# Performance work log

Hardware: AMD Instinct MI355X
Metric: run time of the kernel (lower is better)

## Reference

```python
import jax, jax.numpy as jnp
import numpy as np

B, C, H, W = 8, 512, 64, 128
K = 19          # num_classes
BH, BW = 2, 4   # bin_size
N = BH * BW     # bin_num
CI = C // 2     # feat_inner


def setup_inputs() -> dict:
    ks = jax.random.split(jax.random.key(0), 10)
    def nrm(k, shape, s=0.02):
        return jax.random.normal(k, shape, jnp.float32) * s
    return {
        "x": jax.random.normal(ks[0], (B, C, H, W), jnp.float32),
        "conv_cam_w": nrm(ks[1], (K, C)),
        "conv_cam_b": jnp.zeros((K,), jnp.float32),
        "gcn_w1": nrm(ks[2], (N, N), 0.1),
        "gcn_a": jnp.full((N,), 0.25, jnp.float32),
        "gcn_w2": nrm(ks[3], (C, C)),
        "fuse_w": nrm(ks[4], (1, N), 0.1),
        "fuse_b": jnp.zeros((1,), jnp.float32),
        "relu_a": jnp.full((1,), 0.25, jnp.float32),
        "q_w": nrm(ks[5], (CI, C)),
        "q_b": jnp.zeros((CI,), jnp.float32),
        "k_w": nrm(ks[6], (CI, C)),
        "k_b": jnp.zeros((CI,), jnp.float32),
        "v_w": nrm(ks[7], (CI, C)),
        "v_b": jnp.zeros((CI,), jnp.float32),
        "out_w": nrm(ks[8], (C, CI)),
        "bn_gamma": jnp.ones((C,), jnp.float32),
        "bn_beta": jnp.zeros((C,), jnp.float32),
        "out_a": jnp.full((C,), 0.25, jnp.float32),
    }


def _prelu(x, a):
    return jnp.maximum(x, 0) + a * jnp.minimum(x, 0)


def _split(t):
    # [b, cc, H, W] -> [b, N, rh*rw, cc]  (patch_split)
    b, cc = t.shape[0], t.shape[1]
    rh, rw = H // BH, W // BW
    t = t.reshape(b, cc, BH, rh, BW, rw).transpose(0, 2, 4, 3, 5, 1)
    return t.reshape(b, N, rh * rw, cc)


def _caam(x, conv_cam_w, conv_cam_b, gcn_w1, gcn_a, gcn_w2, fuse_w, fuse_b,
          relu_a, q_w, q_b, k_w, k_b, v_w, v_b, out_w, bn_gamma, bn_beta, out_a):
    b = x.shape[0]
    rh, rw = H // BH, W // BW
    # CAM (1x1 conv) + adaptive avg pool to bins + sigmoid
    cam = jnp.einsum('bchw,kc->bkhw', x, conv_cam_w) + conv_cam_b[None, :, None, None]
    cls_score = jax.nn.sigmoid(cam.reshape(b, K, BH, rh, BW, rw).mean((3, 5)))  # [b,K,BH,BW]
    cam_p = _split(cam)   # [b,N,P,K]
    x_p = _split(x)       # [b,N,P,C]
    bin_conf = cls_score.reshape(b, K, N).transpose(0, 2, 1)[..., None]  # [b,N,K,1]
    pix_conf = jax.nn.softmax(cam_p, axis=2)
    local = jnp.einsum('bnpk,bnpc->bnkc', pix_conf, x_p) * bin_conf  # [b,N,K,C]
    # GCN: conv1 over bin dim, PReLU(residual), Linear over channels
    t = jnp.einsum('nm,bmkc->bnkc', gcn_w1, local)
    t = _prelu(t + local, gcn_a[None, :, None, None])
    local = jnp.einsum('bnkc,dc->bnkd', t, gcn_w2)
    # fuse bins -> single global descriptor, PReLU(1)
    glob = jnp.einsum('on,bnkc->bokc', fuse_w, local) + fuse_b[None, :, None, None]  # [b,1,K,C]
    glob = _prelu(glob[:, 0], relu_a[0])  # [b,K,C]
    # QKV attention over bins (key/value over K class slots)
    q = jnp.einsum('bnpc,ic->bnpi', x_p, q_w) + q_b       # [b,N,P,CI]
    key = jnp.einsum('bnkc,ic->bnki', local, k_w) + k_b   # [b,N,K,CI]
    val = jnp.einsum('bkc,ic->bki', glob, v_w) + v_b      # [b,K,CI] (shared across bins)
    aff = jax.nn.softmax(jnp.einsum('bnpi,bnki->bnpk', q, key), axis=-1)
    out = jnp.einsum('bnpk,bki->bnpi', aff, val)          # [b,N,P,CI]
    # patch_recover -> [b,CI,H,W]
    out = out.reshape(b, BH, BW, rh, rw, CI).transpose(0, 5, 1, 3, 2, 4).reshape(b, CI, H, W)
    # conv_out: 1x1 conv (no bias) + BatchNorm2d (batch stats) + PReLU(C)
    y = jnp.einsum('bihw,ci->bchw', out, out_w)
    mu = y.mean((0, 2, 3), keepdims=True)
    var = y.var((0, 2, 3), keepdims=True)
    y = (y - mu) * jax.lax.rsqrt(var + 1e-5)
    y = y * bn_gamma[None, :, None, None] + bn_beta[None, :, None, None]
    y = _prelu(y, out_a[None, :, None, None])
    return x + y


def reference(x, conv_cam_w, conv_cam_b, gcn_w1, gcn_a, gcn_w2, fuse_w, fuse_b,
              relu_a, q_w, q_b, k_w, k_b, v_w, v_b, out_w, bn_gamma, bn_beta, out_a):
    return _caam(x, conv_cam_w, conv_cam_b, gcn_w1, gcn_a, gcn_w2, fuse_w, fuse_b,
                 relu_a, q_w, q_b, k_w, k_b, v_w, v_b, out_w, bn_gamma, bn_beta, out_a)
```

## Files before the change

### kernel.cpp

```cpp
#include <hip/hip_runtime.h>
#include <cstdint>
#include <cstddef>

#define B_ 8
#define C_ 512
#define H_ 64
#define W_ 128
#define HW_ 8192
#define K_ 19
#define N_ 8
#define P_ 1024
#define CI_ 256

typedef unsigned short u16;
typedef unsigned int u32;
typedef __attribute__((ext_vector_type(8))) short bf16x8;
typedef __attribute__((ext_vector_type(4))) float f32x4;

__device__ __forceinline__ u16 f2bf(float f) {
  u32 u = __float_as_uint(f);
  u32 r = (u + 0x7FFFu + ((u >> 16) & 1u)) >> 16;
  return (u16)r;
}
__device__ __forceinline__ float bf2f(u16 h) {
  return __uint_as_float(((u32)h) << 16);
}

__device__ __forceinline__ void gload16(const u16* g, u16* l) {
  __builtin_amdgcn_global_load_lds(
      (const __attribute__((address_space(1))) unsigned int*)g,
      (__attribute__((address_space(3))) unsigned int*)l, 16, 0, 0);
}

__device__ __forceinline__ void stage128(const u16* __restrict__ src, size_t ld, int k0,
                                         u16* lds, int wave, int lane) {
  int rsub = lane >> 3;
  int swz = ((lane & 7) ^ rsub) << 3;
#pragma unroll
  for (int i = 0; i < 4; i++) {
    int rowbase = wave * 8 + i * 32;
    gload16(src + (size_t)(rowbase + rsub) * ld + k0 + swz, lds + rowbase * 64);
  }
}
__device__ __forceinline__ void stage32(const u16* __restrict__ src, size_t ld, int k0,
                                        u16* lds, int wave, int lane) {
  int rsub = lane >> 3;
  int swz = ((lane & 7) ^ rsub) << 3;
  int rowbase = wave * 8;
  gload16(src + (size_t)(rowbase + rsub) * ld + k0 + swz, lds + rowbase * 64);
}
__device__ __forceinline__ bf16x8 frag(const u16* lds, int row, int qbyte) {
  return *(const bf16x8*)((const char*)lds + row * 128 + (qbyte ^ ((row & 7) << 4)));
}

__device__ __forceinline__ float blockSum256(float v, float* red4) {
#pragma unroll
  for (int o = 32; o > 0; o >>= 1) v += __shfl_down(v, o, 64);
  __syncthreads();
  if ((threadIdx.x & 63) == 0) red4[threadIdx.x >> 6] = v;
  __syncthreads();
  return red4[0] + red4[1] + red4[2] + red4[3];
}

__device__ __forceinline__ float blockMax256(float v, float* red4) {
#pragma unroll
  for (int o = 32; o > 0; o >>= 1) v = fmaxf(v, __shfl_down(v, o, 64));
  __syncthreads();
  if ((threadIdx.x & 63) == 0) red4[threadIdx.x >> 6] = v;
  __syncthreads();
  return fmaxf(fmaxf(red4[0], red4[1]), fmaxf(red4[2], red4[3]));
}

__device__ __forceinline__ void cvt4(const float* __restrict__ s, u16* __restrict__ d, int i) {
  float4 v = *(const float4*)&s[(size_t)i * 4];
  ushort4 o;
  o.x = f2bf(v.x); o.y = f2bf(v.y); o.z = f2bf(v.z); o.w = f2bf(v.w);
  *(ushort4*)&d[(size_t)i * 4] = o;
}

__global__ __launch_bounds__(256) void xpose_prep_kernel(const float* __restrict__ x,
                                                         u16* __restrict__ xt,
                                                         const float* __restrict__ qw,
                                                         const float* __restrict__ ow,
                                                         const float* __restrict__ kw,
                                                         const float* __restrict__ gw2,
                                                         const float* __restrict__ camw,
                                                         u16* __restrict__ qwbf,
                                                         u16* __restrict__ owbf,
                                                         u16* __restrict__ kwbf,
                                                         u16* __restrict__ gw2bf,
                                                         u16* __restrict__ camwbf,
                                                         float* __restrict__ sums,
                                                         float* __restrict__ tpad) {
  __shared__ float tile[64][65];
  int bid = blockIdx.x;
  int tid = threadIdx.x;
  if (bid >= 8192) {
    int pb = bid - 8192;
    if (pb < 128) {
      cvt4(qw, qwbf, pb * 256 + tid);
    } else if (pb < 256) {
      cvt4(ow, owbf, (pb - 128) * 256 + tid);
    } else if (pb < 384) {
      cvt4(kw, kwbf, (pb - 256) * 256 + tid);
    } else if (pb < 640) {
      cvt4(gw2, gw2bf, (pb - 384) * 256 + tid);
    } else if (pb < 656) {
      int i = (pb - 640) * 256 + tid;
      if (i * 4 < K_ * C_) {
        cvt4(camw, camwbf, i);
      } else {
        ushort4 z; z.x = 0; z.y = 0; z.z = 0; z.w = 0;
        *(ushort4*)&camwbf[(size_t)i * 4] = z;
      }
    } else if (pb == 656) {
      float4 z; z.x = 0.f; z.y = 0.f; z.z = 0.f; z.w = 0.f;
      *(float4*)&sums[tid * 4] = z;
    } else {
      int i = (pb - 657) * 256 + tid;
      float4 z; z.x = 0.f; z.y = 0.f; z.z = 0.f; z.w = 0.f;
      *(float4*)&tpad[(size_t)i * 4] = z;
    }
    return;
  }
  int hw0 = (bid & 127) << 6;
  int c0 = ((bid >> 7) & 7) << 6;
  int b = bid >> 10;
  int r = tid >> 4;
  int col4 = (tid & 15) << 2;
  const float* xb = x + ((size_t)b * C_ + c0) * HW_ + hw0;
#pragma unroll
  for (int it = 0; it < 4; it++) {
    int rr = r + it * 16;
    float4 v = *(const float4*)&xb[(size_t)rr * HW_ + col4];
    tile[rr][col4 + 0] = v.x;
    tile[rr][col4 + 1] = v.y;
    tile[rr][col4 + 2] = v.z;
    tile[rr][col4 + 3] = v.w;
  }
  __syncthreads();
  u16* xo = xt + ((size_t)b * HW_ + hw0) * C_ + c0;
#pragma unroll
  for (int it = 0; it < 4; it++) {
    int hwr = r + it * 16;
    ushort4 o;
    o.x = f2bf(tile[col4 + 0][hwr]);
    o.y = f2bf(tile[col4 + 1][hwr]);
    o.z = f2bf(tile[col4 + 2][hwr]);
    o.w = f2bf(tile[col4 + 3][hwr]);
    *(ushort4*)&xo[(size_t)hwr * C_ + col4] = o;
  }
}

__global__ __launch_bounds__(256) void gemm_cam_kernel(const u16* __restrict__ A,
                                                       const u16* __restrict__ Bw,
                                                       const float* __restrict__ bias,
                                                       float* __restrict__ cam) {
  __shared__ __align__(16) u16 As[128 * 64];
  __shared__ __align__(16) u16 Bs[32 * 64];
  int b = blockIdx.y;
  int m0 = blockIdx.x * 128;
  int tid = threadIdx.x;
  int wave = tid >> 6, lane = tid & 63;
  int wm = wave * 32;
  int quad = lane >> 4, l16 = lane & 15;
  const u16* Ab = A + (size_t)b * HW_ * C_ + (size_t)m0 * C_;
  f32x4 acc[2][2] = {};
  for (int k0 = 0; k0 < C_; k0 += 64) {
    __syncthreads();
    stage128(Ab, C_, k0, As, wave, lane);
    stage32(Bw, C_, k0, Bs, wave, lane);
    __syncthreads();
#pragma unroll
    for (int kk = 0; kk < 2; kk++) {
      int qb_ = kk * 64 + quad * 16;
      bf16x8 af[2], bfv[2];
#pragma unroll
      for (int t = 0; t < 2; t++) {
        af[t] = frag(As, wm + t * 16 + l16, qb_);
        bfv[t] = frag(Bs, t * 16 + l16, qb_);
      }
#pragma unroll
      for (int tm = 0; tm < 2; tm++)
#pragma unroll
        for (int tn = 0; tn < 2; tn++)
          acc[tm][tn] = __builtin_amdgcn_mfma_f32_16x16x32_bf16(af[tm], bfv[tn], acc[tm][tn], 0, 0, 0);
    }
  }
  float* C = cam + (size_t)b * K_ * HW_;
#pragma unroll
  for (int tm = 0; tm < 2; tm++) {
    int mm = m0 + wm + tm * 16 + quad * 4;
#pragma unroll
    for (int tn = 0; tn < 2; tn++) {
      int nn = tn * 16 + l16;
      if (nn < K_) {
        float bv = bias[nn];
        f32x4 v = acc[tm][tn];
        v[0] += bv; v[1] += bv; v[2] += bv; v[3] += bv;
        *(f32x4*)&C[(size_t)nn * HW_ + mm] = v;
      }
    }
  }
}

__global__ __launch_bounds__(256) void softcls_kernel(const float* __restrict__ cam,
                                                      float* __restrict__ bconf,
                                                      float* __restrict__ pconf) {
  __shared__ float red4[4];
  int bid = blockIdx.x;
  int k = bid % 19;
  int n = (bid / 19) & 7;
  int b = bid / 152;
  int bh = n >> 2, bw = n & 3;
  const float* base = cam + ((size_t)b * K_ + k) * HW_ + (bh * 32) * W_ + bw * 32;
  float v[4];
  float s = 0.f, mx = -1e30f;
#pragma unroll
  for (int j = 0; j < 4; j++) {
    int p = threadIdx.x + j * 256;
    v[j] = base[(p >> 5) * W_ + (p & 31)];
    s += v[j];
    mx = fmaxf(mx, v[j]);
  }
  float tot = blockSum256(s, red4);
  if (threadIdx.x == 0) {
    float m = tot * (1.f / 1024.f);
    bconf[bid] = 1.f / (1.f + __expf(-m));
  }
  mx = blockMax256(mx, red4);
  float e[4];
  float se = 0.f;
#pragma unroll
  for (int j = 0; j < 4; j++) { e[j] = __expf(v[j] - mx); se += e[j]; }
  se = blockSum256(se, red4);
  float inv = 1.f / se;
  float* outp = pconf + (size_t)bid * P_;
#pragma unroll
  for (int j = 0; j < 4; j++) outp[threadIdx.x + j * 256] = e[j] * inv;
}

__global__ __launch_bounds__(256) void local_part_kernel(const u16* __restrict__ xt,
                                                         const float* __restrict__ pconf,
                                                         float* __restrict__ part) {
  __shared__ __align__(16) float pcl[19 * 256];
  int bid = blockIdx.x;
  int pq = bid & 3;
  int half = (bid >> 2) & 1;
  int n = (bid >> 3) & 7;
  int b = bid >> 6;
  int tid = threadIdx.x;
  int c = half * 256 + tid;
  int bh = n >> 2, bw = n & 3;
  const float* pcb = pconf + (size_t)((b * N_ + n) * K_) * P_ + pq * 256;
  for (int e = tid; e < 19 * 64; e += 256) {
    int k = e >> 6, q4 = e & 63;
    *(float4*)&pcl[k * 256 + q4 * 4] = *(const float4*)&pcb[(size_t)k * P_ + q4 * 4];
  }
  __syncthreads();
  float acc[K_];
#pragma unroll
  for (int k = 0; k < K_; k++) acc[k] = 0.f;
  const u16* xb = xt + (size_t)b * HW_ * C_ + c;
  for (int pl0 = 0; pl0 < 256; pl0 += 8) {
    float xv[8];
#pragma unroll
    for (int g = 0; g < 2; g++) {
      int p = pq * 256 + pl0 + g * 4;
      int hw = (bh * 32 + (p >> 5)) * W_ + bw * 32 + (p & 31);
      const u16* xr = xb + (size_t)hw * C_;
#pragma unroll
      for (int j = 0; j < 4; j++) xv[g * 4 + j] = bf2f(xr[(size_t)j * C_]);
    }
#pragma unroll
    for (int k = 0; k < K_; k++) {
      float4 p0 = *(const float4*)&pcl[k * 256 + pl0];
      float4 p1 = *(const float4*)&pcl[k * 256 + pl0 + 4];
      acc[k] += p0.x * xv[0] + p0.y * xv[1] + p0.z * xv[2] + p0.w * xv[3]
              + p1.x * xv[4] + p1.y * xv[5] + p1.z * xv[6] + p1.w * xv[7];
    }
  }
  int row = (b * N_ + n) * K_;
  float* pp = part + ((size_t)pq * 1216 + row) * C_ + c;
#pragma unroll
  for (int k = 0; k < K_; k++) pp[(size_t)k * C_] = acc[k];
}

__global__ __launch_bounds__(256) void t_kernel(const float* __restrict__ part,
                                                const float* __restrict__ bconf,
                                                const float* __restrict__ gw1,
                                                const float* __restrict__ ga,
                                                u16* __restrict__ tbuf) {
  __shared__ float gw1l[64];
  __shared__ float gal[8];
  __shared__ float bcl[8];
  int tid = threadIdx.x;
  int bid = blockIdx.x;
  int half = bid & 1;
  int rem = bid >> 1;
  int k = rem % 19;
  int b = rem / 19;
  if (tid < 64) gw1l[tid] = gw1[tid];
  if (tid < 8) {
    gal[tid] = ga[tid];
    bcl[tid] = bconf[(size_t)(b * 8 + tid) * 19 + k];
  }
  __syncthreads();
  int c = half * 256 + tid;
  float lm[8];
#pragma unroll
  for (int m = 0; m < 8; m++) {
    size_t off = ((size_t)(b * N_ + m) * K_ + k) * C_ + c;
    lm[m] = (part[off] + part[off + (size_t)1216 * 512] +
             part[off + (size_t)2 * 1216 * 512] + part[off + (size_t)3 * 1216 * 512]) * bcl[m];
  }
#pragma unroll
  for (int n = 0; n < 8; n++) {
    float v = lm[n];
#pragma unroll
    for (int m = 0; m < 8; m++) v += gw1l[n * 8 + m] * lm[m];
    float t = fmaxf(v, 0.f) + gal[n] * fminf(v, 0.f);
    tbuf[((size_t)((b * N_ + n) * K_ + k)) * C_ + c] = f2bf(t);
  }
}

template <int KDIM, int NDIM, bool BIAS>
__device__ __forceinline__ void gemm_small_body(int bidx,
                                                const u16* __restrict__ A,
                                                const u16* __restrict__ Bw,
                                                const float* __restrict__ bias,
                                                float* __restrict__ f32out,
                                                u16* __restrict__ bf16out,
                                                u16* As, u16* Bs) {
  constexpr int NT = NDIM / 128;
  int m0 = (bidx / NT) * 128;
  int n0 = (bidx % NT) * 128;
  int tid = threadIdx.x;
  int wave = tid >> 6, lane = tid & 63;
  int wm = (wave >> 1) * 64, wn = (wave & 1) * 64;
  int quad = lane >> 4, l16 = lane & 15;
  const u16* Ab = A + (size_t)m0 * KDIM;
  const u16* Bb = Bw + (size_t)n0 * KDIM;
  f32x4 acc[4][4] = {};
  for (int k0 = 0; k0 < KDIM; k0 += 64) {
    __syncthreads();
    stage128(Ab, KDIM, k0, As, wave, lane);
    stage128(Bb, KDIM, k0, Bs, wave, lane);
    __syncthreads();
#pragma unroll
    for (int kk = 0; kk < 2; kk++) {
      int qb_ = kk * 64 + quad * 16;
      bf16x8 af[4], bfv[4];
#pragma unroll
      for (int t = 0; t < 4; t++) {
        af[t] = frag(As, wm + t * 16 + l16, qb_);
        bfv[t] = frag(Bs, wn + t * 16 + l16, qb_);
      }
#pragma unroll
      for (int tm = 0; tm < 4; tm++)
#pragma unroll
        for (int tn = 0; tn < 4; tn++)
          acc[tm][tn] = __builtin_amdgcn_mfma_f32_16x16x32_bf16(af[tm], bfv[tn], acc[tm][tn], 0, 0, 0);
    }
  }
  float bv[4];
#pragma unroll
  for (int tn = 0; tn < 4; tn++)
    bv[tn] = BIAS ? bias[n0 + wn + tn * 16 + l16] : 0.f;
#pragma unroll
  for (int tm = 0; tm < 4; tm++) {
    int mm = m0 + wm + tm * 16 + quad * 4;
#pragma unroll
    for (int tn = 0; tn < 4; tn++) {
      int nn = n0 + wn + tn * 16 + l16;
#pragma unroll
      for (int reg = 0; reg < 4; reg++) {
        float v = acc[tm][tn][reg] + bv[tn];
        if (f32out) f32out[(size_t)(mm + reg) * NDIM + nn] = v;
        if (bf16out) bf16out[(size_t)(mm + reg) * NDIM + nn] = f2bf(v);
      }
    }
  }
}

template <int KDIM, int NDIM, bool BIAS>
__global__ __launch_bounds__(256) void gemm_small_kernel(const u16* __restrict__ A,
                                                         const u16* __restrict__ Bw,
                                                         const float* __restrict__ bias,
                                                         float* __restrict__ f32out,
                                                         u16* __restrict__ bf16out) {
  __shared__ __align__(16) u16 As[128 * 64];
  __shared__ __align__(16) u16 Bs[128 * 64];
  gemm_small_body<KDIM, NDIM, BIAS>(blockIdx.x, A, Bw, bias, f32out, bf16out, As, Bs);
}

__device__ __forceinline__ void glob_val_body(int bid,
                                              const float* __restrict__ locl2,
                                              const float* __restrict__ fw,
                                              const float* __restrict__ fb,
                                              const float* __restrict__ ra,
                                              const float* __restrict__ vw,
                                              const float* __restrict__ vb,
                                              float* __restrict__ valo,
                                              float* gl) {
  int k = bid % 19;
  int b = bid / 19;
  int tid = threadIdx.x;
  float fwr[8];
#pragma unroll
  for (int m = 0; m < 8; m++) fwr[m] = fw[m];
  float fbv = fb[0], rav = ra[0];
  const float* lb = locl2 + ((size_t)(b * N_) * K_ + k) * C_;
  for (int c = tid; c < C_; c += 256) {
    float v = fbv;
#pragma unroll
    for (int m = 0; m < 8; m++) v += fwr[m] * lb[(size_t)m * K_ * C_ + c];
    gl[c] = fmaxf(v, 0.f) + rav * fminf(v, 0.f);
  }
  __syncthreads();
  int i = tid;
  const float* wr = vw + (size_t)i * C_;
  float s = vb[i];
  for (int c4 = 0; c4 < C_; c4 += 4) {
    float4 wv = *(const float4*)&wr[c4];
    float4 tv = *(const float4*)&gl[c4];
    s += wv.x * tv.x + wv.y * tv.y + wv.z * tv.z + wv.w * tv.w;
  }
  valo[(size_t)bid * CI_ + i] = s;
}

__global__ __launch_bounds__(256) void small2_globval_kernel(const u16* __restrict__ A,
                                                             const u16* __restrict__ Bw,
                                                             const float* __restrict__ bias,
                                                             float* __restrict__ keyo,
                                                             const float* __restrict__ locl2,
                                                             const float* __restrict__ fw,
                                                             const float* __restrict__ fb,
                                                             const float* __restrict__ ra,
                                                             const float* __restrict__ vw,
                                                             const float* __restrict__ vb,
                                                             float* __restrict__ valo) {
  __shared__ __align__(16) u16 As[128 * 64];
  __shared__ __align__(16) u16 Bs[128 * 64];
  if (blockIdx.x < 20) {
    gemm_small_body<512, 256, true>(blockIdx.x, A, Bw, bias, keyo, nullptr, As, Bs);
  } else {
    glob_val_body(blockIdx.x - 20, locl2, fw, fb, ra, vw, vb, valo, (float*)As);
  }
}

template <int KDIM, int NDIM, bool TRANS_OUT, bool BIAS, bool OUTBF16, bool BNSTAT>
__global__ __launch_bounds__(256) void gemm_big_kernel(const u16* __restrict__ A,
                                                       const u16* __restrict__ Bw,
                                                       const float* __restrict__ bias,
                                                       void* __restrict__ Cout,
                                                       float* __restrict__ sums,
                                                       float* __restrict__ sumsq) {
  __shared__ __align__(16) u16 As[128 * 64];
  __shared__ __align__(16) u16 Bs[128 * 64];
  constexpr int NT = NDIM / 128;
  int b = blockIdx.y;
  int d = blockIdx.x;
  int xcd = d & 7;
  int j = d >> 3;
  int m0 = (xcd + 8 * (j / NT)) * 128;
  int n0 = (j % NT) * 128;
  int tid = threadIdx.x;
  int wave = tid >> 6, lane = tid & 63;
  int wm = (wave >> 1) * 64, wn = (wave & 1) * 64;
  int quad = lane >> 4, l16 = lane & 15;
  const u16* Ab = A + (size_t)b * 8192 * KDIM + (size_t)m0 * KDIM;
  const u16* Bb = Bw + (size_t)n0 * KDIM;
  f32x4 acc[4][4] = {};
  for (int k0 = 0; k0 < KDIM; k0 += 64) {
    __syncthreads();
    stage128(Ab, KDIM, k0, As, wave, lane);
    stage128(Bb, KDIM, k0, Bs, wave, lane);
    __syncthreads();
#pragma unroll
    for (int kk = 0; kk < 2; kk++) {
      int qb_ = kk * 64 + quad * 16;
      bf16x8 af[4], bfv[4];
#pragma unroll
      for (int t = 0; t < 4; t++) {
        af[t] = frag(As, wm + t * 16 + l16, qb_);
        bfv[t] = frag(Bs, wn + t * 16 + l16, qb_);
      }
#pragma unroll
      for (int tm = 0; tm < 4; tm++)
#pragma unroll
        for (int tn = 0; tn < 4; tn++)
          acc[tm][tn] = __builtin_amdgcn_mfma_f32_16x16x32_bf16(af[tm], bfv[tn], acc[tm][tn], 0, 0, 0);
    }
  }
  if constexpr (!TRANS_OUT) {
    float bv[4];
#pragma unroll
    for (int tn = 0; tn < 4; tn++)
      bv[tn] = BIAS ? bias[n0 + wn + tn * 16 + l16] : 0.f;
#pragma unroll
    for (int tm = 0; tm < 4; tm++) {
      int mm = m0 + wm + tm * 16 + quad * 4;
#pragma unroll
      for (int tn = 0; tn < 4; tn++) {
        int nn = n0 + wn + tn * 16 + l16;
        if constexpr (OUTBF16) {
          u16* C = (u16*)Cout + (size_t)b * 8192 * NDIM;
#pragma unroll
          for (int reg = 0; reg < 4; reg++)
            C[(size_t)(mm + reg) * NDIM + nn] = f2bf(acc[tm][tn][reg] + bv[tn]);
        } else {
          float* C = (float*)Cout + (size_t)b * 8192 * NDIM;
#pragma unroll
          for (int reg = 0; reg < 4; reg++)
            C[(size_t)(mm + reg) * NDIM + nn] = acc[tm][tn][reg] + bv[tn];
        }
      }
    }
  } else {
    float* C = (float*)Cout + (size_t)b * NDIM * 8192;
#pragma unroll
    for (int tm = 0; tm < 4; tm++) {
      int mm = m0 + wm + tm * 16 + quad * 4;
#pragma unroll
      for (int tn = 0; tn < 4; tn++) {
        int nn = n0 + wn + tn * 16 + l16;
        *(f32x4*)&C[(size_t)nn * 8192 + mm] = acc[tm][tn];
      }
    }
    if constexpr (BNSTAT) {
#pragma unroll
      for (int tn = 0; tn < 4; tn++) {
        int nn = n0 + wn + tn * 16 + l16;
        float s = 0.f, q = 0.f;
#pragma unroll
        for (int tm = 0; tm < 4; tm++)
#pragma unroll
          for (int reg = 0; reg < 4; reg++) {
            float v = acc[tm][tn][reg];
            s += v;
            q += v * v;
          }
        s += __shfl_xor(s, 16, 64); q += __shfl_xor(q, 16, 64);
        s += __shfl_xor(s, 32, 64); q += __shfl_xor(q, 32, 64);
        if (quad == 0) {
          atomicAdd(&sums[nn], s);
          atomicAdd(&sumsq[nn], q);
        }
      }
    }
  }
}

__global__ __launch_bounds__(256) void attn2_kernel(const u16* __restrict__ q,
                                                    const float* __restrict__ keyo,
                                                    const float* __restrict__ valo,
                                                    u16* __restrict__ obuf) {
  __shared__ float keyl[19 * 256];
  __shared__ float vall[19 * 256];
  __shared__ float aff[128 * 20];
  int bid = blockIdx.x;
  int rg = bid & 7;
  int n = (bid >> 3) & 7;
  int b = bid >> 6;
  int bh = n >> 2, bw = n & 3;
  int tid = threadIdx.x;
  const float* ksrc = keyo + (size_t)((b * 8 + n) * 19) * 256;
  for (int e = tid; e < 19 * 256; e += 256) keyl[e] = ksrc[e];
  __syncthreads();
  if (tid < 128) {
    int r = rg * 4 + (tid >> 5);
    int wc = tid & 31;
    int hw = (bh * 32 + r) * W_ + bw * 32 + wc;
    const u16* qr = q + ((size_t)b * HW_ + hw) * 256;
    float acc[19];
#pragma unroll
    for (int k = 0; k < 19; k++) acc[k] = 0.f;
    for (int i0 = 0; i0 < 256; i0 += 8) {
      uint4 v = *(const uint4*)&qr[i0];
      float f0 = __uint_as_float((v.x & 0xFFFFu) << 16);
      float f1 = __uint_as_float(v.x & 0xFFFF0000u);
      float f2 = __uint_as_float((v.y & 0xFFFFu) << 16);
      float f3 = __uint_as_float(v.y & 0xFFFF0000u);
      float f4 = __uint_as_float((v.z & 0xFFFFu) << 16);
      float f5 = __uint_as_float(v.z & 0xFFFF0000u);
      float f6 = __uint_as_float((v.w & 0xFFFFu) << 16);
      float f7 = __uint_as_float(v.w & 0xFFFF0000u);
#pragma unroll
      for (int k = 0; k < 19; k++) {
        const float* kr = &keyl[k * 256 + i0];
        acc[k] += f0 * kr[0] + f1 * kr[1] + f2 * kr[2] + f3 * kr[3] +
                  f4 * kr[4] + f5 * kr[5] + f6 * kr[6] + f7 * kr[7];
      }
    }
    float mx = -1e30f;
#pragma unroll
    for (int k = 0; k < 19; k++) mx = fmaxf(mx, acc[k]);
    float se = 0.f;
#pragma unroll
    for (int k = 0; k < 19; k++) { acc[k] = __expf(acc[k] - mx); se += acc[k]; }
    float inv = 1.f / se;
#pragma unroll
    for (int k = 0; k < 19; k++) aff[tid * 20 + k] = acc[k] * inv;
  } else {
    const float* vsrc = valo + (size_t)b * 19 * 256;
    for (int e = tid - 128; e < 19 * 256; e += 128) vall[e] = vsrc[e];
  }
  __syncthreads();
  int px = tid & 127;
  int ih = (tid >> 7) * 128;
  int r3 = rg * 4 + (px >> 5);
  int wc3 = px & 31;
  int hw3 = (bh * 32 + r3) * W_ + bw * 32 + wc3;
  float av[19];
#pragma unroll
  for (int k = 0; k < 19; k++) av[k] = aff[px * 20 + k];
  u16* ob = obuf + ((size_t)b * HW_ + hw3) * 256 + ih;
  for (int i0 = 0; i0 < 128; i0 += 16) {
    float o16[16];
#pragma unroll
    for (int j = 0; j < 16; j++) o16[j] = 0.f;
#pragma unroll
    for (int k = 0; k < 19; k++) {
      float a = av[k];
      const float* vr = &vall[k * 256 + ih + i0];
#pragma unroll
      for (int j = 0; j < 16; j++) o16[j] += a * vr[j];
    }
    uint4 w0, w1;
    w0.x = (u32)f2bf(o16[0]) | ((u32)f2bf(o16[1]) << 16);
    w0.y = (u32)f2bf(o16[2]) | ((u32)f2bf(o16[3]) << 16);
    w0.z = (u32)f2bf(o16[4]) | ((u32)f2bf(o16[5]) << 16);
    w0.w = (u32)f2bf(o16[6]) | ((u32)f2bf(o16[7]) << 16);
    w1.x = (u32)f2bf(o16[8]) | ((u32)f2bf(o16[9]) << 16);
    w1.y = (u32)f2bf(o16[10]) | ((u32)f2bf(o16[11]) << 16);
    w1.z = (u32)f2bf(o16[12]) | ((u32)f2bf(o16[13]) << 16);
    w1.w = (u32)f2bf(o16[14]) | ((u32)f2bf(o16[15]) << 16);
    *(uint4*)&ob[i0] = w0;
    *(uint4*)&ob[i0 + 8] = w1;
  }
}

__global__ __launch_bounds__(256) void final_kernel(const float* __restrict__ x,
                                                    const float* __restrict__ sums,
                                                    const float* __restrict__ sumsq,
                                                    const float* __restrict__ gamma,
                                                    const float* __restrict__ beta,
                                                    const float* __restrict__ oa,
                                                    float* __restrict__ out) {
  size_t base = (size_t)blockIdx.x * 4096 + threadIdx.x * 4;
  int c = (int)((base >> 13) & 511);
  const float inv_cnt = 1.f / 65536.f;
  float mu = sums[c] * inv_cnt;
  float var = sumsq[c] * inv_cnt - mu * mu;
  float iv = rsqrtf(var + 1e-5f);
  float sc = gamma[c] * iv;
  float sh = beta[c] - mu * sc;
  float a = oa[c];
#pragma unroll
  for (int jj = 0; jj < 4; jj++) {
    size_t idx = base + (size_t)jj * 1024;
    float4 y = *(float4*)&out[idx];
    float4 xv = *(const float4*)&x[idx];
    float4 r;
    float t;
    t = y.x * sc + sh; r.x = xv.x + fmaxf(t, 0.f) + a * fminf(t, 0.f);
    t = y.y * sc + sh; r.y = xv.y + fmaxf(t, 0.f) + a * fminf(t, 0.f);
    t = y.z * sc + sh; r.z = xv.z + fmaxf(t, 0.f) + a * fminf(t, 0.f);
    t = y.w * sc + sh; r.w = xv.w + fmaxf(t, 0.f) + a * fminf(t, 0.f);
    *(float4*)&out[idx] = r;
  }
}

extern "C" void kernel_launch(void* const* d_in, const int* in_sizes, int n_in,
                              void* d_out, int out_size, void* d_ws, size_t ws_size,
                              hipStream_t stream) {
  const float* x     = (const float*)d_in[0];
  const float* camw  = (const float*)d_in[1];
  const float* camb  = (const float*)d_in[2];
  const float* gw1   = (const float*)d_in[3];
  const float* ga    = (const float*)d_in[4];
  const float* gw2   = (const float*)d_in[5];
  const float* fw    = (const float*)d_in[6];
  const float* fb    = (const float*)d_in[7];
  const float* ra    = (const float*)d_in[8];
  const float* qw    = (const float*)d_in[9];
  const float* qb    = (const float*)d_in[10];
  const float* kw    = (const float*)d_in[11];
  const float* kb    = (const float*)d_in[12];
  const float* vw    = (const float*)d_in[13];
  const float* vb    = (const float*)d_in[14];
  const float* ow    = (const float*)d_in[15];
  const float* gamma = (const float*)d_in[16];
  const float* beta  = (const float*)d_in[17];
  const float* oa    = (const float*)d_in[18];
  float* out = (float*)d_out;
  float* ws = (float*)d_ws;

  float* cam    = ws;
  float* bconf  = cam + 1245184;
  float* pconf  = bconf + 2048;
  float* locl   = pconf + 1245184;
  float* locl2f = locl + 622592;
  float* keyo   = locl2f + 655360;
  float* valo   = keyo + 327680;
  float* sums   = valo + 38912;
  float* sumsq  = sums + 512;
  float* scale  = sumsq + 512;
  float* shift  = scale + 512;
  u16* qwbf   = (u16*)(shift + 512);
  u16* owbf   = qwbf + 131072;
  u16* kwbf   = owbf + 131072;
  u16* gw2bf  = kwbf + 131072;
  u16* camwbf = gw2bf + 262144;
  u16* tbuf   = camwbf + 16384;
  u16* l2bf   = tbuf + 655360;
  u16* xt     = l2bf + 655360;
  u16* obuf   = xt;
  u16* qbuf   = xt + 33554432;
  float* part = (float*)qbuf;

  xpose_prep_kernel<<<8865, 256, 0, stream>>>(x, xt, qw, ow, kw, gw2, camw,
                                              qwbf, owbf, kwbf, gw2bf, camwbf,
                                              sums, (float*)(tbuf + 1216 * 512));
  gemm_cam_kernel<<<dim3(64, 8), 256, 0, stream>>>(xt, camwbf, camb, cam);
  softcls_kernel<<<1216, 256, 0, stream>>>(cam, bconf, pconf);
  local_part_kernel<<<512, 256, 0, stream>>>(xt, pconf, part);
  t_kernel<<<304, 256, 0, stream>>>(part, bconf, gw1, ga, tbuf);
  gemm_small_kernel<512, 512, false>
      <<<40, 256, 0, stream>>>(tbuf, gw2bf, nullptr, locl2f, l2bf);
  small2_globval_kernel<<<172, 256, 0, stream>>>(l2bf, kwbf, kb, keyo,
                                                 locl2f, fw, fb, ra, vw, vb, valo);
  gemm_big_kernel<512, 256, false, true, true, false>
      <<<dim3(128, 8), 256, 0, stream>>>(xt, qwbf, qb, qbuf, nullptr, nullptr);
  attn2_kernel<<<512, 256, 0, stream>>>(qbuf, keyo, valo, obuf);
  gemm_big_kernel<256, 512, true, false, false, true>
      <<<dim3(256, 8), 256, 0, stream>>>(obuf, owbf, nullptr, out, sums, sumsq);
  final_kernel<<<8192, 256, 0, stream>>>(x, sums, sumsq, gamma, beta, oa, out);
}
```

Baseline: 549.3 us.

## Split Q-projection GEMM across small kernels and store conv_out result as bf16

The standalone Q-projection GEMM is cut into four slices of two batches each. Each slice is appended as extra blocks to one of the small, under-occupied kernels in the middle of the pipeline (local_part, t, small gemm, key/globval), so its work overlaps with that serial chain. Separately, the conv_out GEMM now writes y as bf16 instead of fp32, halving that intermediate's write and read traffic for final_kernel. BN statistics are still taken from the fp32 accumulators, but y itself is rounded to bf16 before normalisation, and the workspace layout moves part further out to make room.

```diff
diff --git a/kernel.cpp b/kernel.cpp
--- a/kernel.cpp
+++ b/kernel.cpp
@@ -240,11 +240,135 @@
   for (int j = 0; j < 4; j++) outp[threadIdx.x + j * 256] = e[j] * inv;
 }
 
-__global__ __launch_bounds__(256) void local_part_kernel(const u16* __restrict__ xt,
-                                                         const float* __restrict__ pconf,
-                                                         float* __restrict__ part) {
-  __shared__ __align__(16) float pcl[19 * 256];
-  int bid = blockIdx.x;
+template <int KDIM, int NDIM, bool TRANS_OUT, bool BIAS, bool OUTBF16, bool BNSTAT>
+__device__ __forceinline__ void gemm_big_body(int bx, int b,
+                                              const u16* __restrict__ A,
+                                              const u16* __restrict__ Bw,
+                                              const float* __restrict__ bias,
+                                              void* __restrict__ Cout,
+                                              float* __restrict__ sums,
+                                              float* __restrict__ sumsq,
+                                              u16* As, u16* Bs) {
+  constexpr int NT = NDIM / 128;
+  int xcd = bx & 7;
+  int j = bx >> 3;
+  int m0 = (xcd + 8 * (j / NT)) * 128;
+  int n0 = (j % NT) * 128;
+  int tid = threadIdx.x;
+  int wave = tid >> 6, lane = tid & 63;
+  int wm = (wave >> 1) * 64, wn = (wave & 1) * 64;
+  int quad = lane >> 4, l16 = lane & 15;
+  const u16* Ab = A + (size_t)b * 8192 * KDIM + (size_t)m0 * KDIM;
+  const u16* Bb = Bw + (size_t)n0 * KDIM;
+  f32x4 acc[4][4] = {};
+  for (int k0 = 0; k0 < KDIM; k0 += 64) {
+    __syncthreads();
+    stage128(Ab, KDIM, k0, As, wave, lane);
+    stage128(Bb, KDIM, k0, Bs, wave, lane);
+    __syncthreads();
+#pragma unroll
+    for (int kk = 0; kk < 2; kk++) {
+      int qb_ = kk * 64 + quad * 16;
+      bf16x8 af[4], bfv[4];
+#pragma unroll
+      for (int t = 0; t < 4; t++) {
+        af[t] = frag(As, wm + t * 16 + l16, qb_);
+        bfv[t] = frag(Bs, wn + t * 16 + l16, qb_);
+      }
+#pragma unroll
+      for (int tm = 0; tm < 4; tm++)
+#pragma unroll
+        for (int tn = 0; tn < 4; tn++)
+          acc[tm][tn] = __builtin_amdgcn_mfma_f32_16x16x32_bf16(af[tm], bfv[tn], acc[tm][tn], 0, 0, 0);
+    }
+  }
+  if constexpr (!TRANS_OUT) {
+    float bv[4];
+#pragma unroll
+    for (int tn = 0; tn < 4; tn++)
+      bv[tn] = BIAS ? bias[n0 + wn + tn * 16 + l16] : 0.f;
+#pragma unroll
+    for (int tm = 0; tm < 4; tm++) {
+      int mm = m0 + wm + tm * 16 + quad * 4;
+#pragma unroll
+      for (int tn = 0; tn < 4; tn++) {
+        int nn = n0 + wn + tn * 16 + l16;
+        if constexpr (OUTBF16) {
+          u16* C = (u16*)Cout + (size_t)b * 8192 * NDIM;
+#pragma unroll
+          for (int reg = 0; reg < 4; reg++)
+            C[(size_t)(mm + reg) * NDIM + nn] = f2bf(acc[tm][tn][reg] + bv[tn]);
+        } else {
+          float* C = (float*)Cout + (size_t)b * 8192 * NDIM;
+#pragma unroll
+          for (int reg = 0; reg < 4; reg++)
+            C[(size_t)(mm + reg) * NDIM + nn] = acc[tm][tn][reg] + bv[tn];
+        }
+      }
+    }
+  } else {
+#pragma unroll
+    for (int tm = 0; tm < 4; tm++) {
+      int mm = m0 + wm + tm * 16 + quad * 4;
+#pragma unroll
+      for (int tn = 0; tn < 4; tn++) {
+        int nn = n0 + wn + tn * 16 + l16;
+        if constexpr (OUTBF16) {
+          u16* C = (u16*)Cout + (size_t)b * NDIM * 8192;
+          ushort4 o;
+          o.x = f2bf(acc[tm][tn][0]);
+          o.y = f2bf(acc[tm][tn][1]);
+          o.z = f2bf(acc[tm][tn][2]);
+          o.w = f2bf(acc[tm][tn][3]);
+          *(ushort4*)&C[(size_t)nn * 8192 + mm] = o;
+        } else {
+          float* C = (float*)Cout + (size_t)b * NDIM * 8192;
+          *(f32x4*)&C[(size_t)nn * 8192 + mm] = acc[tm][tn];
+        }
+      }
+    }
+    if constexpr (BNSTAT) {
+#pragma unroll
+      for (int tn = 0; tn < 4; tn++) {
+        int nn = n0 + wn + tn * 16 + l16;
+        float s = 0.f, q = 0.f;
+#pragma unroll
+        for (int tm = 0; tm < 4; tm++)
+#pragma unroll
+          for (int reg = 0; reg < 4; reg++) {
+            float v = acc[tm][tn][reg];
+            s += v;
+            q += v * v;
+          }
+        s += __shfl_xor(s, 16, 64); q += __shfl_xor(q, 16, 64);
+        s += __shfl_xor(s, 32, 64); q += __shfl_xor(q, 32, 64);
+        if (quad == 0) {
+          atomicAdd(&sums[nn], s);
+          atomicAdd(&sumsq[nn], q);
+        }
+      }
+    }
+  }
+}
+
+template <int KDIM, int NDIM, bool TRANS_OUT, bool BIAS, bool OUTBF16, bool BNSTAT>
+__global__ __launch_bounds__(256) void gemm_big_kernel(const u16* __restrict__ A,
+                                                       const u16* __restrict__ Bw,
+                                                       const float* __restrict__ bias,
+                                                       void* __restrict__ Cout,
+                                                       float* __restrict__ sums,
+                                                       float* __restrict__ sumsq) {
+  __shared__ __align__(16) u16 As[128 * 64];
+  __shared__ __align__(16) u16 Bs[128 * 64];
+  gemm_big_body<KDIM, NDIM, TRANS_OUT, BIAS, OUTBF16, BNSTAT>(
+      blockIdx.x, blockIdx.y, A, Bw, bias, Cout, sums, sumsq, As, Bs);
+}
+
+__device__ __forceinline__ void local_part_body(int bid,
+                                                const u16* __restrict__ xt,
+                                                const float* __restrict__ pconf,
+                                                float* __restrict__ part,
+                                                float* pcl) {
   int pq = bid & 3;
   int half = (bid >> 2) & 1;
   int n = (bid >> 3) & 7;
@@ -286,16 +410,46 @@
   for (int k = 0; k < K_; k++) pp[(size_t)k * C_] = acc[k];
 }
 
-__global__ __launch_bounds__(256) void t_kernel(const float* __restrict__ part,
-                                                const float* __restrict__ bconf,
-                                                const float* __restrict__ gw1,
-                                                const float* __restrict__ ga,
-                                                u16* __restrict__ tbuf) {
-  __shared__ float gw1l[64];
-  __shared__ float gal[8];
-  __shared__ float bcl[8];
+__global__ __launch_bounds__(256) void local_part_q_kernel(const u16* __restrict__ xt,
+                                                           const float* __restrict__ pconf,
+                                                           float* __restrict__ part,
+                                                           const u16* __restrict__ qwbf,
+                                                           const float* __restrict__ qb,
+                                                           u16* __restrict__ qbuf) {
+  __shared__ __align__(16) u16 smem[16384];
+  int bid = blockIdx.x;
+  if (bid < 512) {
+    local_part_body(bid, xt, pconf, part, (float*)smem);
+  } else {
+    int cb = bid - 512;
+    gemm_big_body<512, 256, false, true, true, false>(cb & 127, cb >> 7, xt, qwbf, qb,
+                                                      qbuf, nullptr, nullptr,
+                                                      smem, smem + 8192);
+  }
+}
+
+__global__ __launch_bounds__(256) void t_q_kernel(const float* __restrict__ part,
+                                                  const float* __restrict__ bconf,
+                                                  const float* __restrict__ gw1,
+                                                  const float* __restrict__ ga,
+                                                  u16* __restrict__ tbuf,
+                                                  const u16* __restrict__ xt,
+                                                  const u16* __restrict__ qwbf,
+                                                  const float* __restrict__ qb,
+                                                  u16* __restrict__ qbuf) {
+  __shared__ __align__(16) u16 smem[16384];
+  int bid = blockIdx.x;
   int tid = threadIdx.x;
-  int bid = blockIdx.x;
+  if (bid >= 304) {
+    int cb = bid - 304;
+    gemm_big_body<512, 256, false, true, true, false>(cb & 127, 2 + (cb >> 7), xt, qwbf, qb,
+                                                      qbuf, nullptr, nullptr,
+                                                      smem, smem + 8192);
+    return;
+  }
+  float* gw1l = (float*)smem;
+  float* gal = gw1l + 64;
+  float* bcl = gal + 8;
   int half = bid & 1;
   int rem = bid >> 1;
   int k = rem % 19;
@@ -383,15 +537,24 @@
   }
 }
 
-template <int KDIM, int NDIM, bool BIAS>
-__global__ __launch_bounds__(256) void gemm_small_kernel(const u16* __restrict__ A,
-                                                         const u16* __restrict__ Bw,
-                                                         const float* __restrict__ bias,
-                                                         float* __restrict__ f32out,
-                                                         u16* __restrict__ bf16out) {
-  __shared__ __align__(16) u16 As[128 * 64];
-  __shared__ __align__(16) u16 Bs[128 * 64];
-  gemm_small_body<KDIM, NDIM, BIAS>(blockIdx.x, A, Bw, bias, f32out, bf16out, As, Bs);
+__global__ __launch_bounds__(256) void small1_q_kernel(const u16* __restrict__ A,
+                                                       const u16* __restrict__ Bw,
+                                                       float* __restrict__ locl2f,
+                                                       u16* __restrict__ l2bf,
+                                                       const u16* __restrict__ xt,
+                                                       const u16* __restrict__ qwbf,
+                                                       const float* __restrict__ qb,
+                                                       u16* __restrict__ qbuf) {
+  __shared__ __align__(16) u16 smem[16384];
+  int bid = blockIdx.x;
+  if (bid < 40) {
+    gemm_small_body<512, 512, false>(bid, A, Bw, nullptr, locl2f, l2bf, smem, smem + 8192);
+  } else {
+    int cb = bid - 40;
+    gemm_big_body<512, 256, false, true, true, false>(cb & 127, 4 + (cb >> 7), xt, qwbf, qb,
+                                                      qbuf, nullptr, nullptr,
+                                                      smem, smem + 8192);
+  }
 }
 
 __device__ __forceinline__ void glob_val_body(int bid,
@@ -429,126 +592,32 @@
   valo[(size_t)bid * CI_ + i] = s;
 }
 
-__global__ __launch_bounds__(256) void small2_globval_kernel(const u16* __restrict__ A,
-                                                             const u16* __restrict__ Bw,
-                                                             const float* __restrict__ bias,
-                                                             float* __restrict__ keyo,
-                                                             const float* __restrict__ locl2,
-                                                             const float* __restrict__ fw,
-                                                             const float* __restrict__ fb,
-                                                             const float* __restrict__ ra,
-                                                             const float* __restrict__ vw,
-                                                             const float* __restrict__ vb,
-                                                             float* __restrict__ valo) {
-  __shared__ __align__(16) u16 As[128 * 64];
-  __shared__ __align__(16) u16 Bs[128 * 64];
-  if (blockIdx.x < 20) {
-    gemm_small_body<512, 256, true>(blockIdx.x, A, Bw, bias, keyo, nullptr, As, Bs);
-  } else {
-    glob_val_body(blockIdx.x - 20, locl2, fw, fb, ra, vw, vb, valo, (float*)As);
-  }
-}
-
-template <int KDIM, int NDIM, bool TRANS_OUT, bool BIAS, bool OUTBF16, bool BNSTAT>
-__global__ __launch_bounds__(256) void gemm_big_kernel(const u16* __restrict__ A,
-                                                       const u16* __restrict__ Bw,
-                                                       const float* __restrict__ bias,
-                                                       void* __restrict__ Cout,
-                                                       float* __restrict__ sums,
-                                                       float* __restrict__ sumsq) {
-  __shared__ __align__(16) u16 As[128 * 64];
-  __shared__ __align__(16) u16 Bs[128 * 64];
-  constexpr int NT = NDIM / 128;
-  int b = blockIdx.y;
-  int d = blockIdx.x;
-  int xcd = d & 7;
-  int j = d >> 3;
-  int m0 = (xcd + 8 * (j / NT)) * 128;
-  int n0 = (j % NT) * 128;
-  int tid = threadIdx.x;
-  int wave = tid >> 6, lane = tid & 63;
-  int wm = (wave >> 1) * 64, wn = (wave & 1) * 64;
-  int quad = lane >> 4, l16 = lane & 15;
-  const u16* Ab = A + (size_t)b * 8192 * KDIM + (size_t)m0 * KDIM;
-  const u16* Bb = Bw + (size_t)n0 * KDIM;
-  f32x4 acc[4][4] = {};
-  for (int k0 = 0; k0 < KDIM; k0 += 64) {
-    __syncthreads();
-    stage128(Ab, KDIM, k0, As, wave, lane);
-    stage128(Bb, KDIM, k0, Bs, wave, lane);
-    __syncthreads();
-#pragma unroll
-    for (int kk = 0; kk < 2; kk++) {
-      int qb_ = kk * 64 + quad * 16;
-      bf16x8 af[4], bfv[4];
-#pragma unroll
-      for (int t = 0; t < 4; t++) {
-        af[t] = frag(As, wm + t * 16 + l16, qb_);
-        bfv[t] = frag(Bs, wn + t * 16 + l16, qb_);
-      }
-#pragma unroll
-      for (int tm = 0; tm < 4; tm++)
-#pragma unroll
-        for (int tn = 0; tn < 4; tn++)
-          acc[tm][tn] = __builtin_amdgcn_mfma_f32_16x16x32_bf16(af[tm], bfv[tn], acc[tm][tn], 0, 0, 0);
-    }
-  }
-  if constexpr (!TRANS_OUT) {
-    float bv[4];
-#pragma unroll
-    for (int tn = 0; tn < 4; tn++)
-      bv[tn] = BIAS ? bias[n0 + wn + tn * 16 + l16] : 0.f;
-#pragma unroll
-    for (int tm = 0; tm < 4; tm++) {
-      int mm = m0 + wm + tm * 16 + quad * 4;
-#pragma unroll
-      for (int tn = 0; tn < 4; tn++) {
-        int nn = n0 + wn + tn * 16 + l16;
-        if constexpr (OUTBF16) {
-          u16* C = (u16*)Cout + (size_t)b * 8192 * NDIM;
-#pragma unroll
-          for (int reg = 0; reg < 4; reg++)
-            C[(size_t)(mm + reg) * NDIM + nn] = f2bf(acc[tm][tn][reg] + bv[tn]);
-        } else {
-          float* C = (float*)Cout + (size_t)b * 8192 * NDIM;
-#pragma unroll
-          for (int reg = 0; reg < 4; reg++)
-            C[(size_t)(mm + reg) * NDIM + nn] = acc[tm][tn][reg] + bv[tn];
-        }
-      }
-    }
-  } else {
-    float* C = (float*)Cout + (size_t)b * NDIM * 8192;
-#pragma unroll
-    for (int tm = 0; tm < 4; tm++) {
-      int mm = m0 + wm + tm * 16 + quad * 4;
-#pragma unroll
-      for (int tn = 0; tn < 4; tn++) {
-        int nn = n0 + wn + tn * 16 + l16;
-        *(f32x4*)&C[(size_t)nn * 8192 + mm] = acc[tm][tn];
-      }
-    }
-    if constexpr (BNSTAT) {
-#pragma unroll
-      for (int tn = 0; tn < 4; tn++) {
-        int nn = n0 + wn + tn * 16 + l16;
-        float s = 0.f, q = 0.f;
-#pragma unroll
-        for (int tm = 0; tm < 4; tm++)
-#pragma unroll
-          for (int reg = 0; reg < 4; reg++) {
-            float v = acc[tm][tn][reg];
-            s += v;
-            q += v * v;
-          }
-        s += __shfl_xor(s, 16, 64); q += __shfl_xor(q, 16, 64);
-        s += __shfl_xor(s, 32, 64); q += __shfl_xor(q, 32, 64);
-        if (quad == 0) {
-          atomicAdd(&sums[nn], s);
-          atomicAdd(&sumsq[nn], q);
-        }
-      }
-    }
+__global__ __launch_bounds__(256) void small2gv_q_kernel(const u16* __restrict__ A,
+                                                         const u16* __restrict__ Bw,
+                                                         const float* __restrict__ bias,
+                                                         float* __restrict__ keyo,
+                                                         const float* __restrict__ locl2,
+                                                         const float* __restrict__ fw,
+                                                         const float* __restrict__ fb,
+                                                         const float* __restrict__ ra,
+                                                         const float* __restrict__ vw,
+                                                         const float* __restrict__ vb,
+                                                         float* __restrict__ valo,
+                                                         const u16* __restrict__ xt,
+                                                         const u16* __restrict__ qwbf,
+                                                         const float* __restrict__ qb,
+                                                         u16* __restrict__ qbuf) {
+  __shared__ __align__(16) u16 smem[16384];
+  int bid = blockIdx.x;
+  if (bid < 20) {
+    gemm_small_body<512, 256, true>(bid, A, Bw, bias, keyo, nullptr, smem, smem + 8192);
+  } else if (bid < 172) {
+    glob_val_body(bid - 20, locl2, fw, fb, ra, vw, vb, valo, (float*)smem);
+  } else if (bid >= 176) {
+    int cb = bid - 176;
+    gemm_big_body<512, 256, false, true, true, false>(cb & 127, 6 + (cb >> 7), xt, qwbf, qb,
+                                                      qbuf, nullptr, nullptr,
+                                                      smem, smem + 8192);
   }
 }
 
@@ -642,6 +711,7 @@
 }
 
 __global__ __launch_bounds__(256) void final_kernel(const float* __restrict__ x,
+                                                    const u16* __restrict__ ybf,
                                                     const float* __restrict__ sums,
                                                     const float* __restrict__ sumsq,
                                                     const float* __restrict__ gamma,
@@ -660,14 +730,14 @@
 #pragma unroll
   for (int jj = 0; jj < 4; jj++) {
     size_t idx = base + (size_t)jj * 1024;
-    float4 y = *(float4*)&out[idx];
+    ushort4 yv = *(const ushort4*)&ybf[idx];
     float4 xv = *(const float4*)&x[idx];
     float4 r;
     float t;
-    t = y.x * sc + sh; r.x = xv.x + fmaxf(t, 0.f) + a * fminf(t, 0.f);
-    t = y.y * sc + sh; r.y = xv.y + fmaxf(t, 0.f) + a * fminf(t, 0.f);
-    t = y.z * sc + sh; r.z = xv.z + fmaxf(t, 0.f) + a * fminf(t, 0.f);
-    t = y.w * sc + sh; r.w = xv.w + fmaxf(t, 0.f) + a * fminf(t, 0.f);
+    t = bf2f(yv.x) * sc + sh; r.x = xv.x + fmaxf(t, 0.f) + a * fminf(t, 0.f);
+    t = bf2f(yv.y) * sc + sh; r.y = xv.y + fmaxf(t, 0.f) + a * fminf(t, 0.f);
+    t = bf2f(yv.z) * sc + sh; r.z = xv.z + fmaxf(t, 0.f) + a * fminf(t, 0.f);
+    t = bf2f(yv.w) * sc + sh; r.w = xv.w + fmaxf(t, 0.f) + a * fminf(t, 0.f);
     *(float4*)&out[idx] = r;
   }
 }
@@ -718,23 +788,22 @@
   u16* xt     = l2bf + 655360;
   u16* obuf   = xt;
   u16* qbuf   = xt + 33554432;
-  float* part = (float*)qbuf;
+  u16* ybf    = qbuf;
+  float* part = (float*)(qbuf + 33554432);
 
   xpose_prep_kernel<<<8865, 256, 0, stream>>>(x, xt, qw, ow, kw, gw2, camw,
                                               qwbf, owbf, kwbf, gw2bf, camwbf,
                                               sums, (float*)(tbuf + 1216 * 512));
   gemm_cam_kernel<<<dim3(64, 8), 256, 0, stream>>>(xt, camwbf, camb, cam);
   softcls_kernel<<<1216, 256, 0, stream>>>(cam, bconf, pconf);
-  local_part_kernel<<<512, 256, 0, stream>>>(xt, pconf, part);
-  t_kernel<<<304, 256, 0, stream>>>(part, bconf, gw1, ga, tbuf);
-  gemm_small_kernel<512, 512, false>
-      <<<40, 256, 0, stream>>>(tbuf, gw2bf, nullptr, locl2f, l2bf);
-  small2_globval_kernel<<<172, 256, 0, stream>>>(l2bf, kwbf, kb, keyo,
-                                                 locl2f, fw, fb, ra, vw, vb, valo);
-  gemm_big_kernel<512, 256, false, true, true, false>
-      <<<dim3(128, 8), 256, 0, stream>>>(xt, qwbf, qb, qbuf, nullptr, nullptr);
+  local_part_q_kernel<<<768, 256, 0, stream>>>(xt, pconf, part, qwbf, qb, qbuf);
+  t_q_kernel<<<560, 256, 0, stream>>>(part, bconf, gw1, ga, tbuf, xt, qwbf, qb, qbuf);
+  small1_q_kernel<<<296, 256, 0, stream>>>(tbuf, gw2bf, locl2f, l2bf, xt, qwbf, qb, qbuf);
+  small2gv_q_kernel<<<432, 256, 0, stream>>>(l2bf, kwbf, kb, keyo,
+                                             locl2f, fw, fb, ra, vw, vb, valo,
+                                             xt, qwbf, qb, qbuf);
   attn2_kernel<<<512, 256, 0, stream>>>(qbuf, keyo, valo, obuf);
-  gemm_big_kernel<256, 512, true, false, false, true>
-      <<<dim3(256, 8), 256, 0, stream>>>(obuf, owbf, nullptr, out, sums, sumsq);
-  final_kernel<<<8192, 256, 0, stream>>>(x, sums, sumsq, gamma, beta, oa, out);
-}
+  gemm_big_kernel<256, 512, true, false, true, true>
+      <<<dim3(256, 8), 256, 0, stream>>>(obuf, owbf, nullptr, ybf, sums, sumsq);
+  final_kernel<<<8192, 256, 0, stream>>>(x, ybf, sums, sumsq, gamma, beta, oa, out);
+}
```

Result: faster. 527.8 us (-3.9%).
